# Optimization experiments

Measured on AMD Instinct MI355X. Metric: run time of the kernel, lower is better.

Reference implementation:

```python
import jax, jax.numpy as jnp
import numpy as np

R_CUT = 3.0  # CosineCutoff(3.0) from ANI.__init__


def cosine_cutoff(r):
    # 0.5*(cos(pi*r/rc)+1) for r < rc, else 0
    return 0.5 * (jnp.cos(jnp.pi * r / R_CUT) + 1.0) * (r < R_CUT).astype(r.dtype)


def setup_inputs() -> dict:
    key = jax.random.key(0)
    k1, k2, k3, k4 = jax.random.split(key, 4)
    B, A, N, R = 16, 2048, 96, 16
    # pair distances in [0, 4): some pairs beyond the 3.0 cutoff
    r_ij = jax.random.uniform(k1, (B, A, N), dtype=jnp.float32) * 4.0
    mask = (jax.random.uniform(k2, (B, A, N)) < 0.75).astype(jnp.float32)
    # learned parameters: etas ~ U[0.5, 1.5), rss ~ N(0,1) (matching torch defaults,
    # with rss length fixed to n_radius)
    etas = jax.random.uniform(k3, (R,), dtype=jnp.float32) + 0.5
    rss = jax.random.normal(k4, (R,), dtype=jnp.float32)
    return {"r_ij": r_ij, "mask": mask, "etas": etas, "rss": rss}


def reference(r_ij, mask, etas, rss):
    # x: [B, A, N, R] Gaussian RBF exponent
    x = -etas[None, None, None, :] * (r_ij[..., None] - rss[None, None, None, :]) ** 2
    cut = cosine_cutoff(r_ij)[..., None]          # [B, A, N, 1]
    f = jnp.exp(x) * cut * mask[..., None]        # [B, A, N, R]
    return jnp.sum(f, axis=2)                     # [B, A, R]
```

## Files before the change

### kernel.cpp

```cpp
#include <hip/hip_runtime.h>


#define NN 96
#define RR 16

__global__ __launch_bounds__(256) void ani_radial_kernel(
    const float* __restrict__ r_ij,
    const float* __restrict__ mask,
    const float* __restrict__ etas,
    const float* __restrict__ rss,
    float* __restrict__ out)
{
    const int tid  = threadIdx.x;
    const int rowL = tid >> 4;
    const int t    = tid & 15;
    const long long row = (long long)blockIdx.x * 16 + rowL;

    const float LOG2E = 1.4426950408889634f;
    float k[RR], pb[RR], pc[RR];
    #pragma unroll
    for (int r = 0; r < RR; ++r) {
        const float eta = etas[r];
        const float rs  = rss[r];
        k[r]  = -eta * LOG2E;
        pb[r] = -2.0f * k[r] * rs;
        pc[r] = k[r] * rs * rs;
    }

    const float* __restrict__ pr = r_ij + row * NN;
    const float* __restrict__ pm = mask + row * NN;

    float acc[RR];
    #pragma unroll
    for (int r = 0; r < RR; ++r) acc[r] = 0.0f;

    float dd[6], mm[6];
    #pragma unroll
    for (int j = 0; j < 3; ++j) {
        const int n = 32 * j + 2 * t;
        const float2 d2 = *reinterpret_cast<const float2*>(pr + n);
        const float2 m2 = *reinterpret_cast<const float2*>(pm + n);
        dd[2*j]   = d2.x; dd[2*j+1] = d2.y;
        mm[2*j]   = m2.x; mm[2*j+1] = m2.y;
    }

    #pragma unroll
    for (int u = 0; u < 6; ++u) {
        const float d = dd[u];
        const float c = __builtin_amdgcn_cosf(d * 0.16666666666666666f);
        float w = __builtin_fmaf(0.5f, c, 0.5f);
        w = (d < 3.0f) ? w * mm[u] : 0.0f;
        #pragma unroll
        for (int r = 0; r < RR; ++r) {
            const float e = __builtin_fmaf(__builtin_fmaf(k[r], d, pb[r]), d, pc[r]);
            acc[r] = __builtin_fmaf(__builtin_amdgcn_exp2f(e), w, acc[r]);
        }
    }

#define RSTAGE(S, NV)                                                   \
    {                                                                   \
        const bool hi = (t & (S)) != 0;                                 \
        _Pragma("unroll")                                               \
        for (int i = 0; i < (NV) / 2; ++i) {                            \
            const float send = hi ? acc[i] : acc[i + (NV) / 2];         \
            const float recv = __shfl_xor(send, (S), 16);               \
            const float keep = hi ? acc[i + (NV) / 2] : acc[i];         \
            acc[i] = keep + recv;                                       \
        }                                                               \
    }
    RSTAGE(8, 16)
    RSTAGE(4, 8)
    RSTAGE(2, 4)
    RSTAGE(1, 2)
#undef RSTAGE

    out[row * RR + t] = acc[0];
}

extern "C" void kernel_launch(void* const* d_in, const int* in_sizes, int n_in,
                              void* d_out, int out_size, void* d_ws, size_t ws_size,
                              hipStream_t stream) {
    const float* r_ij = (const float*)d_in[0];
    const float* mask = (const float*)d_in[1];
    const float* etas = (const float*)d_in[2];
    const float* rss  = (const float*)d_in[3];
    float* out = (float*)d_out;

    const int totalRows = in_sizes[0] / NN;
    const int grid = totalRows / 16;

    ani_radial_kernel<<<grid, 256, 0, stream>>>(r_ij, mask, etas, rss, out);
}
```

Before: 15.30 us.

## Compact nonzero-weight neighbors into LDS and loop per radial channel

Each 16-lane row group computes cutoff-times-mask weights, then uses ballot and popcount to compact only neighbors with nonzero weight into a shared-memory pool as (distance, weight) pairs. The count is padded to a multiple of four with zero entries. Each thread then owns one radial channel and loops over the compacted list, evaluating exp2 only for surviving neighbors. This drops the per-thread 16-channel accumulators and the xor-shuffle reduction. The trade-off is a block-wide barrier, LDS traffic and a data-dependent loop trip count, in exchange for skipping roughly half of the exp evaluations (masked-out or beyond-cutoff pairs).

```diff
diff --git a/kernel.cpp b/kernel.cpp
--- a/kernel.cpp
+++ b/kernel.cpp
@@ -1,8 +1,10 @@
 #include <hip/hip_runtime.h>
 
 
-#define NN 96
-#define RR 16
+#define NN    96
+#define RR    16
+#define NROWS 16
+#define SLOTS 104
 
 __global__ __launch_bounds__(256) void ani_radial_kernel(
     const float* __restrict__ r_ij,
@@ -11,70 +13,79 @@
     const float* __restrict__ rss,
     float* __restrict__ out)
 {
+    __shared__ float2 pool[NROWS * SLOTS];
+    __shared__ int    cntLds[NROWS];
+
     const int tid  = threadIdx.x;
     const int rowL = tid >> 4;
     const int t    = tid & 15;
-    const long long row = (long long)blockIdx.x * 16 + rowL;
-
-    const float LOG2E = 1.4426950408889634f;
-    float k[RR], pb[RR], pc[RR];
-    #pragma unroll
-    for (int r = 0; r < RR; ++r) {
-        const float eta = etas[r];
-        const float rs  = rss[r];
-        k[r]  = -eta * LOG2E;
-        pb[r] = -2.0f * k[r] * rs;
-        pc[r] = k[r] * rs * rs;
-    }
+    const int g    = (tid >> 4) & 3;
+    const long long row = (long long)blockIdx.x * NROWS + rowL;
 
     const float* __restrict__ pr = r_ij + row * NN;
     const float* __restrict__ pm = mask + row * NN;
 
-    float acc[RR];
-    #pragma unroll
-    for (int r = 0; r < RR; ++r) acc[r] = 0.0f;
-
-    float dd[6], mm[6];
+    float dd[6], mm[6], ww[6];
     #pragma unroll
     for (int j = 0; j < 3; ++j) {
         const int n = 32 * j + 2 * t;
         const float2 d2 = *reinterpret_cast<const float2*>(pr + n);
         const float2 m2 = *reinterpret_cast<const float2*>(pm + n);
-        dd[2*j]   = d2.x; dd[2*j+1] = d2.y;
-        mm[2*j]   = m2.x; mm[2*j+1] = m2.y;
+        dd[2*j] = d2.x; dd[2*j+1] = d2.y;
+        mm[2*j] = m2.x; mm[2*j+1] = m2.y;
     }
-
     #pragma unroll
     for (int u = 0; u < 6; ++u) {
         const float d = dd[u];
         const float c = __builtin_amdgcn_cosf(d * 0.16666666666666666f);
-        float w = __builtin_fmaf(0.5f, c, 0.5f);
-        w = (d < 3.0f) ? w * mm[u] : 0.0f;
-        #pragma unroll
-        for (int r = 0; r < RR; ++r) {
-            const float e = __builtin_fmaf(__builtin_fmaf(k[r], d, pb[r]), d, pc[r]);
-            acc[r] = __builtin_fmaf(__builtin_amdgcn_exp2f(e), w, acc[r]);
-        }
+        const float w = __builtin_fmaf(0.5f, c, 0.5f) * mm[u];
+        ww[u] = (d < 3.0f) ? w : 0.0f;
     }
 
-#define RSTAGE(S, NV)                                                   \
-    {                                                                   \
-        const bool hi = (t & (S)) != 0;                                 \
-        _Pragma("unroll")                                               \
-        for (int i = 0; i < (NV) / 2; ++i) {                            \
-            const float send = hi ? acc[i] : acc[i + (NV) / 2];         \
-            const float recv = __shfl_xor(send, (S), 16);               \
-            const float keep = hi ? acc[i + (NV) / 2] : acc[i];         \
-            acc[i] = keep + recv;                                       \
-        }                                                               \
+    float2* __restrict__ rowPool = pool + rowL * SLOTS;
+    int base = 0;
+    #pragma unroll
+    for (int u = 0; u < 6; ++u) {
+        const bool p = (ww[u] != 0.0f);
+        const unsigned long long bal = __ballot(p);
+        const unsigned bits = (unsigned)((bal >> (g * 16)) & 0xffffull);
+        const int before = __popc(bits & ((1u << t) - 1u));
+        if (p) rowPool[base + before] = make_float2(dd[u], ww[u]);
+        base += __popc(bits);
     }
-    RSTAGE(8, 16)
-    RSTAGE(4, 8)
-    RSTAGE(2, 4)
-    RSTAGE(1, 2)
-#undef RSTAGE
+    if (t < 4) rowPool[base + t] = make_float2(0.0f, 0.0f);
+    if (t == 0) cntLds[rowL] = (base + 3) & ~3;
+    __syncthreads();
 
-    out[row * RR + t] = acc[0];
+    const float LOG2E = 1.4426950408889634f;
+    const float eta = etas[t];
+    const float rs  = rss[t];
+    const float k  = -eta * LOG2E;
+    const float pb = -2.0f * k * rs;
+    const float pc = k * rs * rs;
+
+    const int n = cntLds[rowL];
+    const float4* __restrict__ q = reinterpret_cast<const float4*>(rowPool);
+
+    float a0 = 0.0f, a1 = 0.0f, a2 = 0.0f, a3 = 0.0f;
+    for (int i = 0; i < n; i += 4) {
+        const float4 x = q[(i >> 1)];
+        const float4 y = q[(i >> 1) + 1];
+        a0 = __builtin_fmaf(
+            __builtin_amdgcn_exp2f(__builtin_fmaf(__builtin_fmaf(k, x.x, pb), x.x, pc)),
+            x.y, a0);
+        a1 = __builtin_fmaf(
+            __builtin_amdgcn_exp2f(__builtin_fmaf(__builtin_fmaf(k, x.z, pb), x.z, pc)),
+            x.w, a1);
+        a2 = __builtin_fmaf(
+            __builtin_amdgcn_exp2f(__builtin_fmaf(__builtin_fmaf(k, y.x, pb), y.x, pc)),
+            y.y, a2);
+        a3 = __builtin_fmaf(
+            __builtin_amdgcn_exp2f(__builtin_fmaf(__builtin_fmaf(k, y.z, pb), y.z, pc)),
+            y.w, a3);
+    }
+
+    out[row * RR + t] = (a0 + a1) + (a2 + a3);
 }
 
 extern "C" void kernel_launch(void* const* d_in, const int* in_sizes, int n_in,
@@ -87,7 +98,7 @@
     float* out = (float*)d_out;
 
     const int totalRows = in_sizes[0] / NN;
-    const int grid = totalRows / 16;
+    const int grid = totalRows / NROWS;
 
     ani_radial_kernel<<<grid, 256, 0, stream>>>(r_ij, mask, etas, rss, out);
 }
```

New measurement: 17.51 us. +14.4%, slower.
